# Optimization experiments

Measured on AMD Instinct MI355X. Metric: run time of the kernel, lower is better.

Reference implementation:

```python
import jax, jax.numpy as jnp
import numpy as np
from jax import lax

DIM = 128
HEADS = 8
HEAD_DIM = DIM // HEADS
SR = 2
B, H, W = 2, 80, 80
SCALE = HEAD_DIM ** (-0.5)
BN_EPS = 1e-5


def _conv1x1(x, w, b):
    # x: (B,C,H,W), w: (O,C), b: (O,)
    return jnp.einsum('bchw,oc->bohw', x, w) + b[None, :, None, None]


def setup_inputs() -> dict:
    key = jax.random.key(0)
    ks = jax.random.split(key, 12)
    s = DIM ** -0.5
    x = jax.random.normal(ks[0], (B, DIM, H, W), dtype=jnp.float32)
    q_w = jax.random.normal(ks[1], (DIM, DIM), dtype=jnp.float32) * s
    q_b = jnp.zeros((DIM,), jnp.float32)
    k_w = jax.random.normal(ks[2], (DIM, DIM), dtype=jnp.float32) * s
    k_b = jnp.zeros((DIM,), jnp.float32)
    v_w = jax.random.normal(ks[3], (DIM, DIM), dtype=jnp.float32) * s
    v_b = jnp.zeros((DIM,), jnp.float32)
    sr_w = jax.random.normal(ks[4], (DIM, DIM, SR, SR), dtype=jnp.float32) * (s / SR)
    sr_b = jnp.zeros((DIM,), jnp.float32)
    bn_gamma = jnp.ones((DIM,), jnp.float32)
    bn_beta = jnp.zeros((DIM,), jnp.float32)
    bn_mean = jnp.zeros((DIM,), jnp.float32)
    bn_var = jnp.ones((DIM,), jnp.float32)
    proj_w = jax.random.normal(ks[5], (DIM, DIM), dtype=jnp.float32) * s
    proj_b = jnp.zeros((DIM,), jnp.float32)
    return dict(x=x, q_w=q_w, q_b=q_b, k_w=k_w, k_b=k_b, v_w=v_w, v_b=v_b,
                sr_w=sr_w, sr_b=sr_b, bn_gamma=bn_gamma, bn_beta=bn_beta,
                bn_mean=bn_mean, bn_var=bn_var, proj_w=proj_w, proj_b=proj_b)


def reference(x, q_w, q_b, k_w, k_b, v_w, v_b, sr_w, sr_b,
              bn_gamma, bn_beta, bn_mean, bn_var, proj_w, proj_b):
    b, c, h, w = x.shape
    n = h * w
    # q: (B,h,N,d)
    q = _conv1x1(x, q_w, q_b).reshape(b, HEADS, HEAD_DIM, n).transpose(0, 1, 3, 2)
    # spatial reduction: Conv2d(k=SR, s=SR) + BN(eval) + ReLU
    x_kv = lax.conv_general_dilated(x, sr_w, window_strides=(SR, SR),
                                    padding='VALID',
                                    dimension_numbers=('NCHW', 'OIHW', 'NCHW'))
    x_kv = x_kv + sr_b[None, :, None, None]
    inv = bn_gamma / jnp.sqrt(bn_var + BN_EPS)
    x_kv = x_kv * inv[None, :, None, None] + (bn_beta - bn_mean * inv)[None, :, None, None]
    x_kv = jax.nn.relu(x_kv)
    n_kv = x_kv.shape[2] * x_kv.shape[3]
    k = _conv1x1(x_kv, k_w, k_b).reshape(b, HEADS, HEAD_DIM, n_kv).transpose(0, 1, 3, 2)
    v = _conv1x1(x_kv, v_w, v_b).reshape(b, HEADS, HEAD_DIM, n_kv).transpose(0, 1, 3, 2)
    # explicit attention: (B,h,N,N_kv)
    attn = jnp.einsum('bhnd,bhmd->bhnm', q, k) * SCALE
    attn = jax.nn.softmax(attn, axis=-1)
    out = jnp.einsum('bhnm,bhmd->bhnd', attn, v)  # (B,h,N,d)
    # faithful to source layout: transpose(1,2) then reshape to (B,C,H,W)
    out = out.transpose(0, 2, 1, 3).reshape(b, c, h, w)
    out = _conv1x1(out, proj_w, proj_b)
    return out
```

## Files before the change

kernel.cpp:

```cpp
#include <hip/hip_runtime.h>
#include <hip/hip_bf16.h>
#include <cmath>

#define DIM 128
#define HEADS 8
#define NBATCH 2
#define NQ 6400
#define NKV 1600
#define NC 50
#define BN_EPS 1e-5f
#define LOG2E 1.4426950408889634f

typedef __bf16 bf16_t;
typedef __attribute__((ext_vector_type(8))) __bf16 bf16x8;
typedef __attribute__((ext_vector_type(16))) float f32x16;

union BF8U { bf16x8 v; unsigned u[4]; };

__device__ inline unsigned packbf2(float a, float b) {
  union { __hip_bfloat162 v; unsigned u; } r;
  r.v = __float22bfloat162_rn(make_float2(a, b));
  return r.u;
}

__device__ inline unsigned short f2bf(float v) {
  unsigned u = __float_as_uint(v);
  return (unsigned short)((u + 0x7FFFu + ((u >> 16) & 1u)) >> 16);
}

__global__ __launch_bounds__(256) void mgemm_qsrkv(
    const float* __restrict__ x,
    const float* __restrict__ qw, const float* __restrict__ kw,
    const float* __restrict__ vw, const float* __restrict__ srw,
    const float* __restrict__ q_b, const float* __restrict__ sr_b,
    const float* __restrict__ k_b, const float* __restrict__ v_b,
    const float* __restrict__ bng, const float* __restrict__ bnb,
    const float* __restrict__ bnm, const float* __restrict__ bnv,
    unsigned short* __restrict__ Qb,
    unsigned short* __restrict__ Kp, unsigned short* __restrict__ Vp,
    float sl)
{
  __shared__ __align__(16) unsigned short xs[32][136];
  int t = threadIdx.x;
  int ln = t & 31, hf = (t >> 5) & 1, wid = t >> 6;
  int b = blockIdx.y;
  int o = wid * 32 + ln;

  if (blockIdx.x < 50) {
    int cid = blockIdx.x;
    int s0 = cid * 32;
    int s = s0 + ln;
    int i = s / 40, j = s % 40;
    const float* xb = x + (size_t)b * DIM * NQ;

    f32x16 acc = {};
#pragma unroll
    for (int p = 0; p < 4; ++p) {
      int ky = p >> 1, kx = p & 1;
      const float* xpos = xb + (2 * i + ky) * 80 + (2 * j + kx);
      const float* wrow = srw + (size_t)o * 512 + p;
#pragma unroll
      for (int c0 = 0; c0 < 128; c0 += 16) {
        int cb = c0 + hf * 8;
        BF8U af, bf;
#pragma unroll
        for (int m = 0; m < 4; ++m) {
          af.u[m] = packbf2(xpos[(size_t)(cb + 2 * m) * NQ],
                            xpos[(size_t)(cb + 2 * m + 1) * NQ]);
          bf.u[m] = packbf2(wrow[(size_t)(cb + 2 * m) * 4],
                            wrow[(size_t)(cb + 2 * m + 1) * 4]);
        }
        acc = __builtin_amdgcn_mfma_f32_32x32x16_bf16(af.v, bf.v, acc, 0, 0, 0);
      }
    }
    float bv = sr_b[o];
    float inv = bng[o] / sqrtf(bnv[o] + BN_EPS);
    float b2 = bnb[o] - bnm[o] * inv;
#pragma unroll
    for (int g = 0; g < 4; ++g)
#pragma unroll
      for (int jj = 0; jj < 4; ++jj) {
        int sr = 8 * g + 4 * hf + jj;
        xs[sr][o] = f2bf(fmaxf((acc[4 * g + jj] + bv) * inv + b2, 0.f));
      }
    __syncthreads();

    const unsigned short* ar2 = &xs[ln][hf * 8];
    const float* kwrow = kw + (size_t)o * DIM;
    const float* vwrow = vw + (size_t)o * DIM;
    f32x16 ka = {}, va = {};
#pragma unroll
    for (int c0 = 0; c0 < 128; c0 += 16) {
      int cb = c0 + hf * 8;
      bf16x8 af = *(const bf16x8*)&ar2[c0];
      BF8U kb, vb;
      float4 k0 = *(const float4*)(kwrow + cb);
      float4 k1 = *(const float4*)(kwrow + cb + 4);
      float4 v0 = *(const float4*)(vwrow + cb);
      float4 v1 = *(const float4*)(vwrow + cb + 4);
      kb.u[0] = packbf2(k0.x, k0.y); kb.u[1] = packbf2(k0.z, k0.w);
      kb.u[2] = packbf2(k1.x, k1.y); kb.u[3] = packbf2(k1.z, k1.w);
      vb.u[0] = packbf2(v0.x, v0.y); vb.u[1] = packbf2(v0.z, v0.w);
      vb.u[2] = packbf2(v1.x, v1.y); vb.u[3] = packbf2(v1.z, v1.w);
      ka = __builtin_amdgcn_mfma_f32_32x32x16_bf16(af, kb.v, ka, 0, 0, 0);
      va = __builtin_amdgcn_mfma_f32_32x32x16_bf16(af, vb.v, va, 0, 0, 0);
    }
    int hloc = o >> 4, d = o & 15;
    {
      float kb2 = k_b[o];
      size_t CB = (((size_t)b * HEADS + hloc) * NC + cid) * 512;
#pragma unroll
      for (int g = 0; g < 4; ++g)
#pragma unroll
        for (int jj = 0; jj < 4; ++jj) {
          int sl2 = 8 * g + 4 * hf + jj;
          Kp[CB + sl2 * 16 + d] = f2bf(ka[4 * g + jj] + kb2);
        }
    }
    {
      float vb2 = v_b[o];
      size_t CB = (((size_t)b * HEADS + hloc) * NC + cid) * 1024;
      uint4 w0, w1;
      w0.x = packbf2(va[0] + vb2, va[1] + vb2);
      w0.y = packbf2(va[2] + vb2, va[3] + vb2);
      w0.z = packbf2(va[4] + vb2, va[5] + vb2);
      w0.w = packbf2(va[6] + vb2, va[7] + vb2);
      w1.x = packbf2(va[8] + vb2, va[9] + vb2);
      w1.y = packbf2(va[10] + vb2, va[11] + vb2);
      w1.z = packbf2(va[12] + vb2, va[13] + vb2);
      w1.w = packbf2(va[14] + vb2, va[15] + vb2);
      *(uint4*)&Vp[CB + d * 16 + hf * 8] = w0;
      *(uint4*)&Vp[CB + 512 + d * 16 + hf * 8] = w1;
    }
    {
      int hh = t >> 5, pos = t & 31;
      size_t addr = (((size_t)b * HEADS + hh) * NC + cid) * 1024 + 256 +
                    ((pos & 16) ? 512 : 0) + (pos & 15);
      Vp[addr] = 0x3F80;
    }
  } else {
    int s0 = (blockIdx.x - 50) * 32;
    int s = s0 + ln;
    const float* xcol = x + (size_t)b * DIM * NQ + s;
    const float* qwrow = qw + (size_t)o * DIM;
    f32x16 acc = {};
#pragma unroll
    for (int c0 = 0; c0 < 128; c0 += 16) {
      int cb = c0 + hf * 8;
      BF8U af, bf;
#pragma unroll
      for (int m = 0; m < 4; ++m)
        af.u[m] = packbf2(xcol[(size_t)(cb + 2 * m) * NQ],
                          xcol[(size_t)(cb + 2 * m + 1) * NQ]);
      float4 b0 = *(const float4*)(qwrow + cb);
      float4 b1 = *(const float4*)(qwrow + cb + 4);
      bf.u[0] = packbf2(b0.x, b0.y); bf.u[1] = packbf2(b0.z, b0.w);
      bf.u[2] = packbf2(b1.x, b1.y); bf.u[3] = packbf2(b1.z, b1.w);
      acc = __builtin_amdgcn_mfma_f32_32x32x16_bf16(af.v, bf.v, acc, 0, 0, 0);
    }
    float bv = q_b[o];
#pragma unroll
    for (int g = 0; g < 4; ++g)
#pragma unroll
      for (int jj = 0; jj < 4; ++jj) {
        int sq = s0 + 8 * g + 4 * hf + jj;
        Qb[((size_t)b * NQ + sq) * DIM + o] = f2bf((acc[4 * g + jj] + bv) * sl);
      }
  }
}

__global__ __launch_bounds__(256) void attn_split(
    const bf16_t* __restrict__ Qb, const bf16_t* __restrict__ Kp,
    const bf16_t* __restrict__ Vp, unsigned short* __restrict__ Pb,
    float* __restrict__ Lsum)
{
  const int t = threadIdx.x;
  const int ln = t & 31, hf = (t >> 5) & 1, wid = t >> 6;
  const int h = blockIdx.y;
  const int b = blockIdx.z & 1, half = blockIdx.z >> 1;
  const int q0 = blockIdx.x * 128 + wid * 32;

  bf16x8 qf = *(const bf16x8*)&Qb[((size_t)b * NQ + q0 + ln) * DIM + h * 16 + hf * 8];
  const int bh = b * HEADS + h;
  const bf16_t* kc = &Kp[((size_t)bh * NC + half * 25) * 512 + ln * 16 + hf * 8];
  const bf16_t* vc = &Vp[((size_t)bh * NC + half * 25) * 1024 + ln * 16 + hf * 8];

  f32x16 acc0 = {}, acc1 = {};
  const f32x16 zero = {};

  bf16x8 kf0 = *(const bf16x8*)kc;
  bf16x8 va0 = *(const bf16x8*)vc;
  bf16x8 vb0 = *(const bf16x8*)(vc + 512);
  bf16x8 kf1 = *(const bf16x8*)(kc + 512);
  bf16x8 va1 = *(const bf16x8*)(vc + 1024);
  bf16x8 vb1 = *(const bf16x8*)(vc + 1536);

  f32x16 S0 = __builtin_amdgcn_mfma_f32_32x32x16_bf16(kf0, qf, zero, 0, 0, 0);

  for (int c = 0; c < 25; ++c) {
    int cn = (c + 2 < 25) ? c + 2 : 24;
    bf16x8 kf2 = *(const bf16x8*)(kc + (size_t)cn * 512);
    bf16x8 va2 = *(const bf16x8*)(vc + (size_t)cn * 1024);
    bf16x8 vb2 = *(const bf16x8*)(vc + (size_t)cn * 1024 + 512);

    f32x16 S1 = __builtin_amdgcn_mfma_f32_32x32x16_bf16(kf1, qf, zero, 0, 0, 0);

    BF8U f0, f1;
#pragma unroll
    for (int i = 0; i < 4; ++i) {
      f0.u[i] = packbf2(__builtin_amdgcn_exp2f(S0[2 * i]),
                        __builtin_amdgcn_exp2f(S0[2 * i + 1]));
      f1.u[i] = packbf2(__builtin_amdgcn_exp2f(S0[8 + 2 * i]),
                        __builtin_amdgcn_exp2f(S0[9 + 2 * i]));
    }

    acc0 = __builtin_amdgcn_mfma_f32_32x32x16_bf16(va0, f0.v, acc0, 0, 0, 0);
    acc1 = __builtin_amdgcn_mfma_f32_32x32x16_bf16(vb0, f1.v, acc1, 0, 0, 0);

    S0 = S1;
    kf0 = kf1; va0 = va1; vb0 = vb1;
    kf1 = kf2; va1 = va2; vb1 = vb2;
  }

  f32x16 acc;
#pragma unroll
  for (int i = 0; i < 16; ++i) acc[i] = acc0[i] + acc1[i];

  unsigned short* prow =
      &Pb[(size_t)(half * 2 + b) * (NQ * DIM) + (size_t)(q0 + ln) * DIM + h * 16 + 4 * hf];
  uint2 w0, w1;
  w0.x = packbf2(acc[0], acc[1]); w0.y = packbf2(acc[2], acc[3]);
  w1.x = packbf2(acc[4], acc[5]); w1.y = packbf2(acc[6], acc[7]);
  *(uint2*)&prow[0] = w0;
  *(uint2*)&prow[8] = w1;
  if (!hf)
    Lsum[(size_t)(half * 2 + b) * (HEADS * NQ) + (size_t)h * NQ + q0 + ln] = acc[8];
}

__global__ __launch_bounds__(256) void proj_comb(
    const unsigned short* __restrict__ Pb, const float* __restrict__ Lsum,
    const float* __restrict__ pw, const float* __restrict__ p_b,
    float* __restrict__ Out)
{
  __shared__ __align__(16) unsigned short As[32][136];
  int t = threadIdx.x;
  int b = blockIdx.y;
  int s0 = blockIdx.x * 32;

  {
    int tx = t & 31, cg = t >> 5;
#pragma unroll
    for (int it = 0; it < 16; ++it) {
      int c = cg * 16 + it;
      int f = c * NQ + s0 + tx;
      int n = f >> 7, hh = (f >> 4) & 7;
      float p0 = __uint_as_float((unsigned)Pb[(size_t)b * (NQ * DIM) + f] << 16);
      float p1 = __uint_as_float((unsigned)Pb[(size_t)(2 + b) * (NQ * DIM) + f] << 16);
      float L = Lsum[(size_t)b * (HEADS * NQ) + (size_t)hh * NQ + n] +
                Lsum[(size_t)(2 + b) * (HEADS * NQ) + (size_t)hh * NQ + n];
      As[tx][c] = f2bf((p0 + p1) / L);
    }
  }
  __syncthreads();

  int ln = t & 31, hf = (t >> 5) & 1, wid = t >> 6;
  int o = wid * 32 + ln;
  const float* brow = pw + (size_t)o * DIM;
  const unsigned short* arow = &As[ln][hf * 8];
  f32x16 acc = {};
#pragma unroll
  for (int c0 = 0; c0 < 128; c0 += 16) {
    int cb = c0 + hf * 8;
    bf16x8 af = *(const bf16x8*)&arow[c0];
    BF8U bf;
    float4 b0 = *(const float4*)(brow + cb);
    float4 b1 = *(const float4*)(brow + cb + 4);
    bf.u[0] = packbf2(b0.x, b0.y); bf.u[1] = packbf2(b0.z, b0.w);
    bf.u[2] = packbf2(b1.x, b1.y); bf.u[3] = packbf2(b1.z, b1.w);
    acc = __builtin_amdgcn_mfma_f32_32x32x16_bf16(af, bf.v, acc, 0, 0, 0);
  }
  float bv = p_b[o];
  float* obase = &Out[((size_t)b * DIM + o) * NQ + s0 + 4 * hf];
#pragma unroll
  for (int g = 0; g < 4; ++g) {
    float4 r;
    r.x = acc[4 * g + 0] + bv; r.y = acc[4 * g + 1] + bv;
    r.z = acc[4 * g + 2] + bv; r.w = acc[4 * g + 3] + bv;
    *(float4*)&obase[8 * g] = r;
  }
}

extern "C" void kernel_launch(void* const* d_in, const int* in_sizes, int n_in,
                              void* d_out, int out_size, void* d_ws, size_t ws_size,
                              hipStream_t stream)
{
  const float* x    = (const float*)d_in[0];
  const float* q_w  = (const float*)d_in[1];
  const float* q_b  = (const float*)d_in[2];
  const float* k_w  = (const float*)d_in[3];
  const float* k_b  = (const float*)d_in[4];
  const float* v_w  = (const float*)d_in[5];
  const float* v_b  = (const float*)d_in[6];
  const float* sr_w = (const float*)d_in[7];
  const float* sr_b = (const float*)d_in[8];
  const float* bng  = (const float*)d_in[9];
  const float* bnb  = (const float*)d_in[10];
  const float* bnm  = (const float*)d_in[11];
  const float* bnv  = (const float*)d_in[12];
  const float* p_w  = (const float*)d_in[13];
  const float* p_b  = (const float*)d_in[14];
  float* out = (float*)d_out;

  float* ws = (float*)d_ws;
  bf16_t* Qb   = (bf16_t*)(ws);
  bf16_t* Kp   = (bf16_t*)(ws + 819200);
  bf16_t* Vp   = (bf16_t*)(ws + 1024000);
  float*  Lsum = ws + 1433600;
  bf16_t* Pb   = (bf16_t*)(ws + 1638400);

  const float sl = 0.25f * LOG2E;

  mgemm_qsrkv<<<dim3(250, NBATCH), dim3(256), 0, stream>>>(
      x, q_w, k_w, v_w, sr_w, q_b, sr_b, k_b, v_b, bng, bnb, bnm, bnv,
      (unsigned short*)Qb, (unsigned short*)Kp, (unsigned short*)Vp, sl);

  attn_split<<<dim3(NQ / 128, HEADS, 4), dim3(256), 0, stream>>>(
      Qb, Kp, Vp, (unsigned short*)Pb, Lsum);

  proj_comb<<<dim3(200, NBATCH), dim3(256), 0, stream>>>(
      (const unsigned short*)Pb, Lsum, p_w, p_b, out);
}
```

Measured before the change: 158.6 us.

## Stage x tiles in shared memory as bf16 for SR-conv and Q projection GEMMs

Both branches of the projection kernel now cooperatively load the x tile once into LDS, converting to bf16, instead of having every wave reload and convert the same strided x elements from global memory. The SR conv reorders its reduction to a 512-long K over (channel, ky, kx), so the weight row is read with contiguous float4 loads and each A fragment is a single 16-byte LDS read. This removes redundant global reads from the four waves and the uncoalesced scalar weight loads. In exchange it adds about 33 KB of LDS and an extra barrier, which may reduce occupancy.

New measurement: 155.2 us. 2.2% less time.

```diff
diff --git a/kernel.cpp b/kernel.cpp
--- a/kernel.cpp
+++ b/kernel.cpp
@@ -40,6 +40,7 @@
     unsigned short* __restrict__ Kp, unsigned short* __restrict__ Vp,
     float sl)
 {
+  __shared__ __align__(16) unsigned short xs4[32][520];
   __shared__ __align__(16) unsigned short xs[32][136];
   int t = threadIdx.x;
   int ln = t & 31, hf = (t >> 5) & 1, wid = t >> 6;
@@ -49,29 +50,36 @@
   if (blockIdx.x < 50) {
     int cid = blockIdx.x;
     int s0 = cid * 32;
-    int s = s0 + ln;
-    int i = s / 40, j = s % 40;
-    const float* xb = x + (size_t)b * DIM * NQ;
-
+
+    {
+      int tx = t & 31, g = t >> 5;
+      int s = s0 + tx;
+      int i = s / 40, j = s % 40;
+      const float* xb = x + (size_t)b * DIM * NQ;
+#pragma unroll
+      for (int u = 0; u < 32; ++u) {
+        int idx2 = g * 32 + u;
+        int c = idx2 >> 1, ky = idx2 & 1;
+        const float* src = xb + (size_t)c * NQ + (2 * i + ky) * 80 + 2 * j;
+        float2 vv = *(const float2*)src;
+        *(unsigned*)&xs4[tx][c * 4 + ky * 2] = packbf2(vv.x, vv.y);
+      }
+    }
+    __syncthreads();
+
+    const unsigned short* arow = &xs4[ln][hf * 8];
+    const float* wrow = srw + (size_t)o * 512;
     f32x16 acc = {};
-#pragma unroll
-    for (int p = 0; p < 4; ++p) {
-      int ky = p >> 1, kx = p & 1;
-      const float* xpos = xb + (2 * i + ky) * 80 + (2 * j + kx);
-      const float* wrow = srw + (size_t)o * 512 + p;
-#pragma unroll
-      for (int c0 = 0; c0 < 128; c0 += 16) {
-        int cb = c0 + hf * 8;
-        BF8U af, bf;
-#pragma unroll
-        for (int m = 0; m < 4; ++m) {
-          af.u[m] = packbf2(xpos[(size_t)(cb + 2 * m) * NQ],
-                            xpos[(size_t)(cb + 2 * m + 1) * NQ]);
-          bf.u[m] = packbf2(wrow[(size_t)(cb + 2 * m) * 4],
-                            wrow[(size_t)(cb + 2 * m + 1) * 4]);
-        }
-        acc = __builtin_amdgcn_mfma_f32_32x32x16_bf16(af.v, bf.v, acc, 0, 0, 0);
-      }
+#pragma unroll 8
+    for (int c0 = 0; c0 < 512; c0 += 16) {
+      int cb = c0 + hf * 8;
+      bf16x8 af = *(const bf16x8*)&arow[c0];
+      BF8U bf;
+      float4 w0 = *(const float4*)(wrow + cb);
+      float4 w1 = *(const float4*)(wrow + cb + 4);
+      bf.u[0] = packbf2(w0.x, w0.y); bf.u[1] = packbf2(w0.z, w0.w);
+      bf.u[2] = packbf2(w1.x, w1.y); bf.u[3] = packbf2(w1.z, w1.w);
+      acc = __builtin_amdgcn_mfma_f32_32x32x16_bf16(af, bf.v, acc, 0, 0, 0);
     }
     float bv = sr_b[o];
     float inv = bng[o] / sqrtf(bnv[o] + BN_EPS);
@@ -140,23 +148,33 @@
     }
   } else {
     int s0 = (blockIdx.x - 50) * 32;
-    int s = s0 + ln;
-    const float* xcol = x + (size_t)b * DIM * NQ + s;
+
+    {
+      int tx = t & 31, cg = t >> 5;
+      const float* xb = x + (size_t)b * DIM * NQ + s0 + tx;
+#pragma unroll
+      for (int it = 0; it < 8; ++it) {
+        int c = 2 * cg + 16 * it;
+        float a0 = xb[(size_t)c * NQ];
+        float a1 = xb[(size_t)(c + 1) * NQ];
+        *(unsigned*)&xs[tx][c] = packbf2(a0, a1);
+      }
+    }
+    __syncthreads();
+
+    const unsigned short* arow = &xs[ln][hf * 8];
     const float* qwrow = qw + (size_t)o * DIM;
     f32x16 acc = {};
 #pragma unroll
     for (int c0 = 0; c0 < 128; c0 += 16) {
       int cb = c0 + hf * 8;
-      BF8U af, bf;
-#pragma unroll
-      for (int m = 0; m < 4; ++m)
-        af.u[m] = packbf2(xcol[(size_t)(cb + 2 * m) * NQ],
-                          xcol[(size_t)(cb + 2 * m + 1) * NQ]);
+      bf16x8 af = *(const bf16x8*)&arow[c0];
+      BF8U bf;
       float4 b0 = *(const float4*)(qwrow + cb);
       float4 b1 = *(const float4*)(qwrow + cb + 4);
       bf.u[0] = packbf2(b0.x, b0.y); bf.u[1] = packbf2(b0.z, b0.w);
       bf.u[2] = packbf2(b1.x, b1.y); bf.u[3] = packbf2(b1.z, b1.w);
-      acc = __builtin_amdgcn_mfma_f32_32x32x16_bf16(af.v, bf.v, acc, 0, 0, 0);
+      acc = __builtin_amdgcn_mfma_f32_32x32x16_bf16(af, bf.v, acc, 0, 0, 0);
     }
     float bv = q_b[o];
 #pragma unroll
```
